# Optimization experiments

Measured on AMD Instinct MI355X. Metric: run time of the kernel, lower is better.

Reference implementation:

```python
import jax, jax.numpy as jnp
import numpy as np

N = 30000      # num_nodes
E = 480000     # num_edges
NF = 128       # node_features
EF = 64        # edge_features
HID = 256      # hidden_dim
L = 4          # num_layers
H = 8          # heads
D = HID // H   # per-head dim = 32
SCALE = 0.02


def _ln(x, g, b, eps=1e-5):
    m = x.mean(-1, keepdims=True)
    v = ((x - m) ** 2).mean(-1, keepdims=True)
    return (x - m) * jax.lax.rsqrt(v + eps) * g + b


def _mlp_head(x, W1, b1, W2, b2):
    return jax.nn.sigmoid(jax.nn.relu(x @ W1 + b1) @ W2 + b2)


def setup_inputs() -> dict:
    key = jax.random.key(0)
    ks = jax.random.split(key, 32)
    r = lambda k, shp: SCALE * jax.random.normal(k, shp, dtype=jnp.float32)
    inp = {
        'x': jax.random.normal(ks[0], (N, NF), dtype=jnp.float32),
        'edge_attr': jax.random.normal(ks[1], (E, EF), dtype=jnp.float32),
        'edge_index': jax.random.randint(ks[2], (2, E), 0, N, dtype=jnp.int32),
        # encoders
        'enc_Wn': r(ks[3], (NF, HID)), 'enc_bn': jnp.zeros((HID,), jnp.float32),
        'enc_We': r(ks[4], (EF, HID)), 'enc_be': jnp.zeros((HID,), jnp.float32),
        # stacked TransformerConv params for L layers
        'Wq': r(ks[5], (L, HID, HID)), 'bq': jnp.zeros((L, HID), jnp.float32),
        'Wk': r(ks[6], (L, HID, HID)), 'bk': jnp.zeros((L, HID), jnp.float32),
        'Wv': r(ks[7], (L, HID, HID)), 'bv': jnp.zeros((L, HID), jnp.float32),
        'We': r(ks[8], (L, HID, HID)),  # lin_edge has no bias in PyG
        'Wsk': r(ks[9], (L, HID, HID)), 'bsk': jnp.zeros((L, HID), jnp.float32),
        # shared LayerNorm (module reuses self.norm every layer)
        'ln_g': jnp.ones((HID,), jnp.float32), 'ln_b': jnp.zeros((HID,), jnp.float32),
        # contagion predictor
        'cp_W1': r(ks[10], (HID, HID // 2)), 'cp_b1': jnp.zeros((HID // 2,), jnp.float32),
        'cp_W2': r(ks[11], (HID // 2, 1)), 'cp_b2': jnp.zeros((1,), jnp.float32),
        # systemic risk predictor
        'sp_W1': r(ks[12], (HID, HID // 2)), 'sp_b1': jnp.zeros((HID // 2,), jnp.float32),
        'sp_W2': r(ks[13], (HID // 2, 1)), 'sp_b2': jnp.zeros((1,), jnp.float32),
    }
    return inp


def reference(x, edge_attr, edge_index, enc_Wn, enc_bn, enc_We, enc_be,
              Wq, bq, Wk, bk, Wv, bv, We, Wsk, bsk, ln_g, ln_b,
              cp_W1, cp_b1, cp_W2, cp_b2, sp_W1, sp_b1, sp_W2, sp_b2):
    src, dst = edge_index[0], edge_index[1]
    h = x @ enc_Wn + enc_bn                 # [N,HID]
    e = edge_attr @ enc_We + enc_be         # [E,HID]
    inv_sqrt_d = 1.0 / jnp.sqrt(jnp.asarray(D, h.dtype))
    for l in range(L):
        # TransformerConv: query at dst, key/value at src, edge bias on both k and v
        q = (h @ Wq[l] + bq[l]).reshape(N, H, D)[dst]            # [E,H,D]
        ke = (e @ We[l]).reshape(E, H, D)                        # [E,H,D]
        k = (h @ Wk[l] + bk[l]).reshape(N, H, D)[src] + ke
        v = (h @ Wv[l] + bv[l]).reshape(N, H, D)[src] + ke
        score = (q * k).sum(-1) * inv_sqrt_d                     # [E,H]
        smax = jax.ops.segment_max(score, dst, num_segments=N)   # [N,H]
        p = jnp.exp(score - smax[dst])
        denom = jax.ops.segment_sum(p, dst, num_segments=N)
        alpha = p / (denom[dst] + 1e-16)                         # scatter-softmax
        agg = jax.ops.segment_sum(alpha[..., None] * v, dst, num_segments=N)
        out = agg.reshape(N, HID) + h @ Wsk[l] + bsk[l]          # concat heads + root skip
        h = _ln(h + out, ln_g, ln_b)                             # residual + shared LN (eval: no dropout)
    g = h.mean(0, keepdims=True)                                 # [1,HID] global mean pool
    contagion_risk = _mlp_head(h, cp_W1, cp_b1, cp_W2, cp_b2)    # [N,1]
    systemic_risk = _mlp_head(g, sp_W1, sp_b1, sp_W2, sp_b2)     # [1,1]
    return h, g, contagion_risk, systemic_risk
```

## Files before the change

kernel.cpp:

```cpp
#include <hip/hip_runtime.h>
#include <cstddef>
#include <cstdint>

#define NN 30000
#define EE 480000
#define NFD 128
#define EFD 64
#define HID 256
#define NL 4
#define NH 8

#define DT_BF16 0
#define DT_F32  1
#define DT_EXT  2

#define OFF_WT  ((size_t)65787648)
#define MIN_B   ((size_t)68015872)
#define MIN_A   ((size_t)129455872)

#define WT_ENC 0
#define WT_LAYER(l) (32768 + (size_t)(l) * 262144)
#define WT_CP1 (32768 + (size_t)1048576)

typedef short bf16x8 __attribute__((ext_vector_type(8)));
typedef unsigned short us8 __attribute__((ext_vector_type(8)));
typedef float f32x4 __attribute__((ext_vector_type(4)));

__device__ __forceinline__ float bf2f(unsigned short u) {
  union { unsigned int i; float f; } v; v.i = ((unsigned int)u) << 16; return v.f;
}
__device__ __forceinline__ unsigned short f2bf(float f) {
  union { float f; unsigned int i; } v; v.f = f;
  unsigned int i = v.i;
  return (unsigned short)((i + 0x7FFFu + ((i >> 16) & 1u)) >> 16);
}
struct F4 { float x, y, z, w; };
__device__ __forceinline__ F4 load4bf(const unsigned short* p) {
  ushort4 u = *reinterpret_cast<const ushort4*>(p);
  F4 f; f.x = bf2f(u.x); f.y = bf2f(u.y); f.z = bf2f(u.z); f.w = bf2f(u.w);
  return f;
}
__device__ __forceinline__ F4 load4f(const float* p) {
  float4 t = *reinterpret_cast<const float4*>(p);
  F4 f; f.x = t.x; f.y = t.y; f.z = t.z; f.w = t.w; return f;
}
__device__ __forceinline__ F4 load4any(const void* p, size_t idx, int f32) {
  return f32 ? load4f((const float*)p + idx) : load4bf((const unsigned short*)p + idx);
}
__device__ __forceinline__ float load1any(const void* p, size_t idx, int f32) {
  return f32 ? ((const float*)p)[idx] : bf2f(((const unsigned short*)p)[idx]);
}
__device__ __forceinline__ void store1any(void* p, size_t idx, float v, int f32) {
  if (f32) ((float*)p)[idx] = v; else ((unsigned short*)p)[idx] = f2bf(v);
}

__global__ void probe_dtype(const void* __restrict__ ln_g, int* __restrict__ flag) {
  unsigned int u = *(const unsigned int*)ln_g;
  *flag = ((u & 0xFFFFu) == 0u) ? 1 : 0;
}

__global__ void wt_build(const void* __restrict__ enc_Wn,
                         const void* __restrict__ Wq, const void* __restrict__ Wk,
                         const void* __restrict__ Wv, const void* __restrict__ Wsk,
                         const void* __restrict__ cp_W1,
                         unsigned short* __restrict__ Wt, const int* __restrict__ flagp)
{
  const int f = *flagp;
  size_t idx = (size_t)blockIdx.x * 256 + threadIdx.x;
  if (idx < 32768) {
    int n = idx >> 7, k = idx & 127;
    Wt[WT_ENC + idx] = f2bf(load1any(enc_Wn, (size_t)k * 256 + n, f));
  } else if (idx < 32768 + 1048576) {
    size_t off = idx - 32768;
    int l = off >> 18;
    int which = (off >> 16) & 3;
    size_t e = off & 65535;
    int n = e >> 8, k = e & 255;
    const void* W = (which == 0) ? Wq : (which == 1) ? Wk : (which == 2) ? Wv : Wsk;
    Wt[idx] = f2bf(load1any(W, (size_t)l * 65536 + (size_t)k * 256 + n, f));
  } else if (idx < 32768 + 1048576 + 32768) {
    size_t e = idx - 32768 - 1048576;
    int n = e >> 8, k = e & 255;
    Wt[idx] = f2bf(load1any(cp_W1, (size_t)k * 128 + n, f));
  }
}

template<bool OUT_F32, bool RELU>
__global__ __launch_bounds__(256) void mfma_gemm(
    const void* __restrict__ Av, int aMode,
    const unsigned short* __restrict__ Bt,
    const void* __restrict__ biasv, size_t biasEl, int biasMode,
    void* __restrict__ Cv, int ldC, int cOff,
    int M, int K, const int* __restrict__ flagp)
{
  const int f = *flagp;
  const int aF32 = (aMode == DT_EXT) ? f : aMode;
  const int biF32 = (biasMode == DT_EXT) ? f : biasMode;

  __shared__ unsigned short Al[128][40];
  __shared__ unsigned short Bl[64][40];
  const int bm = blockIdx.x * 128;
  const int bn = blockIdx.y * 64;
  const int tid = threadIdx.x;
  const int wv = tid >> 6, lane = tid & 63;
  const int l16 = lane & 15, quad = lane >> 4;

  f32x4 acc[2][4];
#pragma unroll
  for (int i = 0; i < 2; i++)
#pragma unroll
    for (int j = 0; j < 4; j++) acc[i][j] = (f32x4){0.f, 0.f, 0.f, 0.f};

  const int ar = tid >> 1;
  const int ah = (tid & 1) << 4;
  const int bnr = tid >> 2;
  const int bk8 = (tid & 3) << 3;

  for (int k0 = 0; k0 < K; k0 += 32) {
    us8 w0, w1;
    int gr = bm + ar;
    if (gr < M) {
      if (!aF32) {
        const unsigned short* ap = (const unsigned short*)Av + (size_t)gr * K + k0 + ah;
        w0 = *(const us8*)ap;
        w1 = *(const us8*)(ap + 8);
      } else {
        const float* ap = (const float*)Av + (size_t)gr * K + k0 + ah;
        float4 u0 = *(const float4*)ap;
        float4 u1 = *(const float4*)(ap + 4);
        float4 u2 = *(const float4*)(ap + 8);
        float4 u3 = *(const float4*)(ap + 12);
        w0[0] = f2bf(u0.x); w0[1] = f2bf(u0.y); w0[2] = f2bf(u0.z); w0[3] = f2bf(u0.w);
        w0[4] = f2bf(u1.x); w0[5] = f2bf(u1.y); w0[6] = f2bf(u1.z); w0[7] = f2bf(u1.w);
        w1[0] = f2bf(u2.x); w1[1] = f2bf(u2.y); w1[2] = f2bf(u2.z); w1[3] = f2bf(u2.w);
        w1[4] = f2bf(u3.x); w1[5] = f2bf(u3.y); w1[6] = f2bf(u3.z); w1[7] = f2bf(u3.w);
      }
    } else {
      w0 = (us8)0; w1 = (us8)0;
    }
    *(us8*)&Al[ar][ah] = w0;
    *(us8*)&Al[ar][ah + 8] = w1;
    *(us8*)&Bl[bnr][bk8] = *(const us8*)&Bt[(size_t)(bn + bnr) * K + k0 + bk8];
    __syncthreads();

    bf16x8 a0 = *(const bf16x8*)&Al[wv * 32 + l16][quad * 8];
    bf16x8 a1 = *(const bf16x8*)&Al[wv * 32 + 16 + l16][quad * 8];
#pragma unroll
    for (int tn = 0; tn < 4; tn++) {
      bf16x8 b = *(const bf16x8*)&Bl[tn * 16 + l16][quad * 8];
      acc[0][tn] = __builtin_amdgcn_mfma_f32_16x16x32_bf16(a0, b, acc[0][tn], 0, 0, 0);
      acc[1][tn] = __builtin_amdgcn_mfma_f32_16x16x32_bf16(a1, b, acc[1][tn], 0, 0, 0);
    }
    __syncthreads();
  }

#pragma unroll
  for (int tm = 0; tm < 2; tm++) {
#pragma unroll
    for (int tn = 0; tn < 4; tn++) {
      int col = bn + tn * 16 + l16;
      float bias = load1any(biasv, biasEl + col, biF32);
#pragma unroll
      for (int r = 0; r < 4; r++) {
        int row = bm + wv * 32 + tm * 16 + quad * 4 + r;
        if (row < M) {
          float v = acc[tm][tn][r] + bias;
          if (RELU) v = fmaxf(v, 0.f);
          size_t off = (size_t)row * ldC + cOff + col;
          if (OUT_F32) ((float*)Cv)[off] = v;
          else ((unsigned short*)Cv)[off] = f2bf(v);
        }
      }
    }
  }
}

__global__ __launch_bounds__(256) void mfma_gemm_qkvs(
    const unsigned short* __restrict__ A,
    const unsigned short* __restrict__ Bt,
    const void* __restrict__ bq, const void* __restrict__ bk,
    const void* __restrict__ bv, const void* __restrict__ bsk, size_t biasEl,
    unsigned short* __restrict__ Qb, unsigned short* __restrict__ KVb,
    unsigned short* __restrict__ Sb,
    int M, const int* __restrict__ flagp)
{
  const int f = *flagp;
  __shared__ unsigned short Al[128][40];
  __shared__ unsigned short Bl[64][40];
  const int bm = blockIdx.x * 128;
  const int bnG = blockIdx.y * 64;
  const int which = bnG >> 8;
  const int bn = bnG & 255;
  const int tid = threadIdx.x;
  const int wv = tid >> 6, lane = tid & 63;
  const int l16 = lane & 15, quad = lane >> 4;

  f32x4 acc[2][4];
#pragma unroll
  for (int i = 0; i < 2; i++)
#pragma unroll
    for (int j = 0; j < 4; j++) acc[i][j] = (f32x4){0.f, 0.f, 0.f, 0.f};

  const int ar = tid >> 1;
  const int ah = (tid & 1) << 4;
  const int bnr = tid >> 2;
  const int bk8 = (tid & 3) << 3;
  const unsigned short* Bbase = Bt + (size_t)which * 65536;

  for (int k0 = 0; k0 < HID; k0 += 32) {
    us8 w0, w1;
    int gr = bm + ar;
    if (gr < M) {
      const unsigned short* ap = A + (size_t)gr * HID + k0 + ah;
      w0 = *(const us8*)ap;
      w1 = *(const us8*)(ap + 8);
    } else {
      w0 = (us8)0; w1 = (us8)0;
    }
    *(us8*)&Al[ar][ah] = w0;
    *(us8*)&Al[ar][ah + 8] = w1;
    *(us8*)&Bl[bnr][bk8] = *(const us8*)&Bbase[(size_t)(bn + bnr) * HID + k0 + bk8];
    __syncthreads();

    bf16x8 a0 = *(const bf16x8*)&Al[wv * 32 + l16][quad * 8];
    bf16x8 a1 = *(const bf16x8*)&Al[wv * 32 + 16 + l16][quad * 8];
#pragma unroll
    for (int tn = 0; tn < 4; tn++) {
      bf16x8 b = *(const bf16x8*)&Bl[tn * 16 + l16][quad * 8];
      acc[0][tn] = __builtin_amdgcn_mfma_f32_16x16x32_bf16(a0, b, acc[0][tn], 0, 0, 0);
      acc[1][tn] = __builtin_amdgcn_mfma_f32_16x16x32_bf16(a1, b, acc[1][tn], 0, 0, 0);
    }
    __syncthreads();
  }

  const void* biasv = (which == 0) ? bq : (which == 1) ? bk : (which == 2) ? bv : bsk;
  unsigned short* out = (which == 0) ? Qb : (which == 3) ? Sb : KVb;
  const int ldC = (which == 1 || which == 2) ? 512 : 256;
  const int cOff = (which == 2) ? 256 : 0;

#pragma unroll
  for (int tm = 0; tm < 2; tm++) {
#pragma unroll
    for (int tn = 0; tn < 4; tn++) {
      int col = bn + tn * 16 + l16;
      float bias = load1any(biasv, biasEl + col, f);
#pragma unroll
      for (int r = 0; r < 4; r++) {
        int row = bm + wv * 32 + tm * 16 + quad * 4 + r;
        if (row < M)
          out[(size_t)row * ldC + cOff + col] = f2bf(acc[tm][tn][r] + bias);
      }
    }
  }
}

__global__ void fold_kernel(const void* __restrict__ enc_We,
                            const void* __restrict__ enc_be,
                            const void* __restrict__ We_all,
                            float* __restrict__ Mfold, const int* __restrict__ flagp)
{
  const int f = *flagp;
  int idx = blockIdx.x * blockDim.x + threadIdx.x;
  if (idx >= NL * 65 * HID) return;
  int l = idx / (65 * HID);
  int rc = idx - l * 65 * HID;
  int row = rc >> 8;
  int col = rc & 255;
  size_t Wbase = (size_t)l * HID * HID;
  float acc = 0.f;
  if (row < 64) {
    for (int k = 0; k < HID; k++)
      acc += load1any(enc_We, (size_t)row * HID + k, f) * load1any(We_all, Wbase + (size_t)k * HID + col, f);
  } else {
    for (int k = 0; k < HID; k++)
      acc += load1any(enc_be, k, f) * load1any(We_all, Wbase + (size_t)k * HID + col, f);
  }
  Mfold[idx] = acc;
}

__global__ void hist_kernel(const int* __restrict__ dst, int* __restrict__ rp) {
  int e = blockIdx.x * 256 + threadIdx.x;
  if (e < EE) atomicAdd(&rp[dst[e]], 1);
}

__global__ __launch_bounds__(1024) void scan_kernel(int* __restrict__ rp) {
  __shared__ int part[1024];
  int t = threadIdx.x;
  int base = t * 30;
  int loc[30];
  int sum = 0;
#pragma unroll
  for (int i = 0; i < 30; i++) {
    int idx = base + i;
    int v = (idx < NN) ? rp[idx] : 0;
    loc[i] = v; sum += v;
  }
  part[t] = sum;
  __syncthreads();
  for (int off = 1; off < 1024; off <<= 1) {
    int v = (t >= off) ? part[t - off] : 0;
    __syncthreads();
    part[t] += v;
    __syncthreads();
  }
  int run = (t == 0) ? 0 : part[t - 1];
#pragma unroll
  for (int i = 0; i < 30; i++) {
    int idx = base + i;
    if (idx < NN) { rp[idx] = run; run += loc[i]; }
    else if (idx == NN) { rp[NN] = run; }
  }
}

__global__ void scatter_kernel(const int* __restrict__ src, const int* __restrict__ dst,
                               const int* __restrict__ rp, int* __restrict__ cnt2,
                               int2* __restrict__ sed) {
  int e = blockIdx.x * 256 + threadIdx.x;
  if (e >= EE) return;
  int d = dst[e];
  int pos = rp[d] + atomicAdd(&cnt2[d], 1);
  int2 v; v.x = src[e]; v.y = e;
  sed[pos] = v;
}

__global__ void ea_build(const int2* __restrict__ sed, const void* __restrict__ edge_attr,
                         unsigned short* __restrict__ ea_srt, const int* __restrict__ flagp) {
  const int f = *flagp;
  int gid = blockIdx.x * 256 + threadIdx.x;
  int pos = gid >> 4;
  int sub = (gid & 15) * 4;
  int e = sed[pos].y;
  F4 v = load4any(edge_attr, (size_t)e * EFD + sub, f);
  ushort4 o; o.x = f2bf(v.x); o.y = f2bf(v.y); o.z = f2bf(v.z); o.w = f2bf(v.w);
  *reinterpret_cast<ushort4*>(ea_srt + (size_t)pos * EFD + sub) = o;
}

template<bool SORTED>
__global__ __launch_bounds__(256, 8) void edge_fused(
    const int* __restrict__ rp, const int2* __restrict__ sed,
    const unsigned short* __restrict__ Qb, const unsigned short* __restrict__ KV,
    const unsigned short* __restrict__ ea_srt,
    const void* __restrict__ edge_attr,
    const float* __restrict__ Mf,
    const unsigned short* __restrict__ Sb,
    unsigned short* __restrict__ hb,
    const void* __restrict__ ln_g, const void* __restrict__ ln_b,
    const int* __restrict__ flagp)
{
  __shared__ float wl[4][8][68];
  const int f = *flagp;
  const int wv = __builtin_amdgcn_readfirstlane(threadIdx.x >> 6);
  const int nw = blockIdx.x * 4 + wv;
  const int lane = threadIdx.x & 63;
  const int hd = lane >> 3;
  const int j = lane & 7;
  const int jb = j << 3;
  const int c4 = lane * 4;

  const size_t rowb = (size_t)nw * HID;
  F4 q4 = load4bf(Qb + rowb + c4);

  float t8[8];
  {
    float q32[32];
#pragma unroll
    for (int i = 0; i < 8; i++) {
      F4 t = load4bf(Qb + rowb + hd * 32 + i * 4);
      q32[i * 4 + 0] = t.x; q32[i * 4 + 1] = t.y; q32[i * 4 + 2] = t.z; q32[i * 4 + 3] = t.w;
    }
#pragma unroll
    for (int kk = 0; kk < 8; kk++) {
      const float* Mrow = Mf + (size_t)(jb + kk) * HID + hd * 32;
      float a = 0.f;
#pragma unroll
      for (int cc = 0; cc < 8; cc++) {
        float4 m4 = *reinterpret_cast<const float4*>(Mrow + cc * 4);
        a = fmaf(m4.x, q32[cc * 4 + 0], a);
        a = fmaf(m4.y, q32[cc * 4 + 1], a);
        a = fmaf(m4.z, q32[cc * 4 + 2], a);
        a = fmaf(m4.w, q32[cc * 4 + 3], a);
      }
      t8[kk] = a;
    }
  }
  float s0;
  {
    F4 b4 = load4f(Mf + (size_t)64 * HID + c4);
    s0 = q4.x * b4.x + q4.y * b4.y + q4.z * b4.z + q4.w * b4.w;
    s0 += __shfl_xor(s0, 1);
    s0 += __shfl_xor(s0, 2);
    s0 += __shfl_xor(s0, 4);
  }

  float accv[4] = {0.f, 0.f, 0.f, 0.f};
  float wacc[8] = {0.f, 0.f, 0.f, 0.f, 0.f, 0.f, 0.f, 0.f};
  float den = 0.f;
  const int beg = rp[nw], end = rp[nw + 1];

  if (beg < end) {
    const float scl = 0.17677669529663687f;
    int tA = beg;
    int tB = (beg + 1 < end) ? beg + 1 : beg;
    int sA = sed[tA].x;
    int sB = sed[tB].x;
    const unsigned short* kvp;
    kvp = KV + (size_t)sA * 512;
    F4 kA = load4bf(kvp + c4);
    F4 vA = load4bf(kvp + 256 + c4);
    kvp = KV + (size_t)sB * 512;
    F4 kB = load4bf(kvp + c4);
    F4 vB = load4bf(kvp + 256 + c4);
    float eaA, eaB;
    if (SORTED) {
      eaA = bf2f(ea_srt[(size_t)tA * EFD + lane]);
      eaB = bf2f(ea_srt[(size_t)tB * EFD + lane]);
    } else {
      eaA = load1any(edge_attr, (size_t)sed[tA].y * EFD + lane, f);
      eaB = load1any(edge_attr, (size_t)sed[tB].y * EFD + lane, f);
    }
    int tC = (beg + 2 < end) ? beg + 2 : beg;
    int tD = (beg + 3 < end) ? beg + 3 : beg;
    int sC = sed[tC].x;
    int sD = sed[tD].x;

    for (int t = beg; t < end; t += 2) {
      kvp = KV + (size_t)sC * 512;
      F4 kC = load4bf(kvp + c4);
      F4 vC = load4bf(kvp + 256 + c4);
      kvp = KV + (size_t)sD * 512;
      F4 kD = load4bf(kvp + c4);
      F4 vD = load4bf(kvp + 256 + c4);
      float eaC, eaD;
      if (SORTED) {
        eaC = bf2f(ea_srt[(size_t)tC * EFD + lane]);
        eaD = bf2f(ea_srt[(size_t)tD * EFD + lane]);
      } else {
        eaC = load1any(edge_attr, (size_t)sed[tC].y * EFD + lane, f);
        eaD = load1any(edge_attr, (size_t)sed[tD].y * EFD + lane, f);
      }
      int tE = (t + 4 < end) ? t + 4 : beg;
      int tF = (t + 5 < end) ? t + 5 : beg;
      int sE = sed[tE].x;
      int sF = sed[tF].x;

      float mB = (t + 1 < end) ? 1.f : 0.f;
      float pA, pB;
      {
        float rB = q4.x * kB.x + q4.y * kB.y + q4.z * kB.z + q4.w * kB.w;
        float eB[8];
#pragma unroll
        for (int i = 0; i < 8; i++) {
          eB[i] = __shfl(eaB, jb + i, 64);
          rB = fmaf(eB[i], t8[i], rB);
        }
        rB += __shfl_xor(rB, 1);
        rB += __shfl_xor(rB, 2);
        rB += __shfl_xor(rB, 4);
        float scB = fminf(fmaxf((rB + s0) * scl, -30.f), 30.f);
        pB = mB * __expf(scB);
        accv[0] = fmaf(pB, vB.x, accv[0]);
        accv[1] = fmaf(pB, vB.y, accv[1]);
        accv[2] = fmaf(pB, vB.z, accv[2]);
        accv[3] = fmaf(pB, vB.w, accv[3]);
#pragma unroll
        for (int i = 0; i < 8; i++) wacc[i] = fmaf(pB, eB[i], wacc[i]);
      }
      {
        float rA = q4.x * kA.x + q4.y * kA.y + q4.z * kA.z + q4.w * kA.w;
        float eA[8];
#pragma unroll
        for (int i = 0; i < 8; i++) {
          eA[i] = __shfl(eaA, jb + i, 64);
          rA = fmaf(eA[i], t8[i], rA);
        }
        rA += __shfl_xor(rA, 1);
        rA += __shfl_xor(rA, 2);
        rA += __shfl_xor(rA, 4);
        float scA = fminf(fmaxf((rA + s0) * scl, -30.f), 30.f);
        pA = __expf(scA);
        accv[0] = fmaf(pA, vA.x, accv[0]);
        accv[1] = fmaf(pA, vA.y, accv[1]);
        accv[2] = fmaf(pA, vA.z, accv[2]);
        accv[3] = fmaf(pA, vA.w, accv[3]);
#pragma unroll
        for (int i = 0; i < 8; i++) wacc[i] = fmaf(pA, eA[i], wacc[i]);
      }
      den += pA + pB;
      kA = kC; vA = vC; eaA = eaC;
      kB = kD; vB = vD; eaB = eaD;
      tC = tE; tD = tF; sC = sE; sD = sF;
    }
  }

#pragma unroll
  for (int i = 0; i < 8; i++) wl[wv][hd][jb + i] = wacc[i];
  __syncthreads();

  float ke0 = 0.f, ke1 = 0.f, ke2 = 0.f, ke3 = 0.f;
#pragma unroll 8
  for (int k = 0; k < 64; k++) {
    float w = wl[wv][hd][k];
    float4 m4 = *reinterpret_cast<const float4*>(Mf + (size_t)k * HID + c4);
    ke0 = fmaf(w, m4.x, ke0);
    ke1 = fmaf(w, m4.y, ke1);
    ke2 = fmaf(w, m4.z, ke2);
    ke3 = fmaf(w, m4.w, ke3);
  }

  float invden = 1.f / (den + 1e-16f);
  float sel = (end > beg) ? 1.f : 0.f;
  __builtin_amdgcn_sched_barrier(0);
  F4 b4 = load4f(Mf + (size_t)64 * HID + c4);
  F4 s4 = load4bf(Sb + rowb + c4);
  F4 hh = load4bf(hb + rowb + c4);
  float r0 = hh.x + sel * ((accv[0] + ke0) * invden + b4.x) + s4.x;
  float r1 = hh.y + sel * ((accv[1] + ke1) * invden + b4.y) + s4.y;
  float r2 = hh.z + sel * ((accv[2] + ke2) * invden + b4.z) + s4.z;
  float r3 = hh.w + sel * ((accv[3] + ke3) * invden + b4.w) + s4.w;

  float sum = r0 + r1 + r2 + r3;
#pragma unroll
  for (int o = 1; o < 64; o <<= 1) sum += __shfl_xor(sum, o);
  float mean = sum * (1.f / HID);
  float d0 = r0 - mean, d1 = r1 - mean, d2 = r2 - mean, d3 = r3 - mean;
  float vs = d0 * d0 + d1 * d1 + d2 * d2 + d3 * d3;
#pragma unroll
  for (int o = 1; o < 64; o <<= 1) vs += __shfl_xor(vs, o);
  float rstd = rsqrtf(vs * (1.f / HID) + 1e-5f);
  ushort4 o4;
  o4.x = f2bf(d0 * rstd * load1any(ln_g, c4 + 0, f) + load1any(ln_b, c4 + 0, f));
  o4.y = f2bf(d1 * rstd * load1any(ln_g, c4 + 1, f) + load1any(ln_b, c4 + 1, f));
  o4.z = f2bf(d2 * rstd * load1any(ln_g, c4 + 2, f) + load1any(ln_b, c4 + 2, f));
  o4.w = f2bf(d3 * rstd * load1any(ln_g, c4 + 3, f) + load1any(ln_b, c4 + 3, f));
  *reinterpret_cast<ushort4*>(hb + rowb + c4) = o4;
}

__global__ void copy_h_out(const unsigned short* __restrict__ h, void* __restrict__ out,
                           const int* __restrict__ flagp) {
  const int f = *flagp;
  int i = blockIdx.x * 256 + threadIdx.x;
  store1any(out, i, bf2f(h[i]), f);
}

__global__ void colsum_kernel(const unsigned short* __restrict__ h, float* __restrict__ gsum) {
  int c = threadIdx.x;
  float s = 0.f;
  for (int r = blockIdx.x; r < NN; r += gridDim.x) s += bf2f(h[(size_t)r * HID + c]);
  atomicAdd(&gsum[c], s);
}

__global__ void write_g_kernel(const float* __restrict__ gsum, void* __restrict__ out,
                               const int* __restrict__ flagp) {
  const int f = *flagp;
  int c = threadIdx.x;
  store1any(out, (size_t)NN * HID + c, gsum[c] * (1.f / NN), f);
}

__global__ __launch_bounds__(256) void cp2_kernel(
    const float* __restrict__ hid, const void* __restrict__ W2,
    const void* __restrict__ b2, void* __restrict__ out,
    const int* __restrict__ flagp)
{
  const int f = *flagp;
  int nw = (blockIdx.x << 2) + (threadIdx.x >> 6);
  if (nw >= NN) return;
  int lane = threadIdx.x & 63;
  const float* hr = hid + (size_t)nw * 128;
  float s = hr[lane * 2] * load1any(W2, lane * 2, f) + hr[lane * 2 + 1] * load1any(W2, lane * 2 + 1, f);
#pragma unroll
  for (int o = 1; o < 64; o <<= 1) s += __shfl_xor(s, o);
  if (lane == 0) {
    float xv = s + load1any(b2, 0, f);
    store1any(out, (size_t)NN * HID + HID + nw, 1.f / (1.f + __expf(-xv)), f);
  }
}

__global__ __launch_bounds__(128) void sys_kernel(
    const float* __restrict__ gsum,
    const void* __restrict__ W1, const void* __restrict__ b1,
    const void* __restrict__ W2, const void* __restrict__ b2,
    void* __restrict__ out, const int* __restrict__ flagp)
{
  const int f = *flagp;
  __shared__ float red[2];
  int j = threadIdx.x;
  float acc = load1any(b1, j, f);
  const float invN = 1.f / NN;
  for (int k = 0; k < HID; k++) acc = fmaf(gsum[k] * invN, load1any(W1, (size_t)k * 128 + j, f), acc);
  float v = fmaxf(acc, 0.f) * load1any(W2, j, f);
#pragma unroll
  for (int o = 1; o < 64; o <<= 1) v += __shfl_xor(v, o);
  if ((j & 63) == 0) red[j >> 6] = v;
  __syncthreads();
  if (j == 0) {
    float xv = red[0] + red[1] + load1any(b2, 0, f);
    store1any(out, (size_t)NN * HID + HID + NN, 1.f / (1.f + __expf(-xv)), f);
  }
}

__global__ void diag_kernel(float* __restrict__ out, float v, int n4) {
  int i = blockIdx.x * 256 + threadIdx.x;
  if (i < n4) out[i] = (i == 0) ? v : 0.f;
}

extern "C" void kernel_launch(void* const* d_in, const int* in_sizes, int n_in,
                              void* d_out, int out_size, void* d_ws, size_t ws_size,
                              hipStream_t stream)
{
  (void)in_sizes; (void)n_in;

  if (ws_size < MIN_B) {
    diag_kernel<<<(out_size / 2 + 255) / 256, 256, 0, stream>>>(
        (float*)d_out, (float)(ws_size >> 20), out_size / 2);
    return;
  }
  const bool planA = (ws_size >= MIN_A);

  const void* x         = d_in[0];
  const void* edge_attr = d_in[1];
  const int*  edge_index= (const int*)d_in[2];
  const void* enc_Wn = d_in[3];
  const void* enc_bn = d_in[4];
  const void* enc_We = d_in[5];
  const void* enc_be = d_in[6];
  const void* Wq  = d_in[7];
  const void* bq  = d_in[8];
  const void* Wk  = d_in[9];
  const void* bk  = d_in[10];
  const void* Wv  = d_in[11];
  const void* bvv = d_in[12];
  const void* We  = d_in[13];
  const void* Wsk = d_in[14];
  const void* bsk = d_in[15];
  const void* ln_g = d_in[16];
  const void* ln_b = d_in[17];
  const void* cp_W1 = d_in[18];
  const void* cp_b1 = d_in[19];
  const void* cp_W2 = d_in[20];
  const void* cp_b2 = d_in[21];
  const void* sp_W1 = d_in[22];
  const void* sp_b1 = d_in[23];
  const void* sp_W2 = d_in[24];
  const void* sp_b2 = d_in[25];

  char* ws = (char*)d_ws;
  unsigned short* hb  = (unsigned short*)(ws + 0);
  unsigned short* Sb  = (unsigned short*)(ws + 15360000);
  unsigned short* KVb = (unsigned short*)(ws + 30720000);
  int2*  sed   = (int2*)(ws + 61440000);
  int*   rp    = (int*)(ws + 65280000);
  int*   cnt2  = (int*)(ws + 65400064);
  float* Mfold = (float*)(ws + 65520128);
  float* gsum  = (float*)(ws + 65786368);
  int*   flagp = (int*)(ws + 65787392);
  unsigned short* Wt = (unsigned short*)(ws + OFF_WT);
  unsigned short* ea_srt = (unsigned short*)(ws + MIN_B);
  unsigned short* Qb = (unsigned short*)d_out;
  float* cph = (float*)(ws + 15360000);

  const int* src = edge_index;
  const int* dst = edge_index + EE;

  probe_dtype<<<1, 1, 0, stream>>>(ln_g, flagp);
  wt_build<<<(1114112 + 255) / 256, 256, 0, stream>>>(enc_Wn, Wq, Wk, Wv, Wsk, cp_W1, Wt, flagp);
  fold_kernel<<<(NL * 65 * HID + 255) / 256, 256, 0, stream>>>(enc_We, enc_be, We, Mfold, flagp);

  hipMemsetAsync(rp, 0, 120064, stream);
  hipMemsetAsync(cnt2, 0, 120064, stream);
  hist_kernel<<<(EE + 255) / 256, 256, 0, stream>>>(dst, rp);
  scan_kernel<<<1, 1024, 0, stream>>>(rp);
  scatter_kernel<<<(EE + 255) / 256, 256, 0, stream>>>(src, dst, rp, cnt2, sed);
  if (planA) {
    ea_build<<<EE * 16 / 256, 256, 0, stream>>>(sed, edge_attr, ea_srt, flagp);
  }

  const int gx = (NN + 127) / 128;
  {
    dim3 g(gx, 4);
    mfma_gemm<false, false><<<g, 256, 0, stream>>>(
        x, DT_EXT, Wt + WT_ENC, enc_bn, 0, DT_EXT, hb, HID, 0, NN, NFD, flagp);
  }

  for (int l = 0; l < NL; l++) {
    size_t bo = (size_t)l * HID;
    dim3 gQ(gx, 16);
    mfma_gemm_qkvs<<<gQ, 256, 0, stream>>>(
        hb, Wt + WT_LAYER(l), bq, bk, bvv, bsk, bo, Qb, KVb, Sb, NN, flagp);
    const float* Mf = Mfold + (size_t)l * 65 * HID;
    if (planA) {
      edge_fused<true><<<NN / 4, 256, 0, stream>>>(
          rp, sed, Qb, KVb, ea_srt, edge_attr, Mf, Sb, hb, ln_g, ln_b, flagp);
    } else {
      edge_fused<false><<<NN / 4, 256, 0, stream>>>(
          rp, sed, Qb, KVb, ea_srt, edge_attr, Mf, Sb, hb, ln_g, ln_b, flagp);
    }
  }

  copy_h_out<<<NN, 256, 0, stream>>>(hb, d_out, flagp);
  hipMemsetAsync(gsum, 0, HID * 4, stream);
  colsum_kernel<<<256, 256, 0, stream>>>(hb, gsum);
  write_g_kernel<<<1, 256, 0, stream>>>(gsum, d_out, flagp);

  {
    dim3 g(gx, 2);
    mfma_gemm<true, true><<<g, 256, 0, stream>>>(
        hb, DT_BF16, Wt + WT_CP1, cp_b1, 0, DT_EXT, cph, 128, 0, NN, HID, flagp);
  }
  cp2_kernel<<<NN / 4, 256, 0, stream>>>(cph, cp_W2, cp_b2, d_out, flagp);
  sys_kernel<<<1, 128, 0, stream>>>(gsum, sp_W1, sp_b1, sp_W2, sp_b2, d_out, flagp);
}
```

Measured before the change: 2.351 ms.

## Rework edge loop: one-ahead prefetch, vector edge-attr loads, scalarized indices

Replaces the two-edges-per-iteration, four-deep register prefetch pipeline in the attention aggregation loop with a simpler ping-pong loop that prefetches only the next edge. Each lane now loads its 8 edge-attribute values directly as one 16-byte vector instead of broadcasting them across lanes with eight shuffles. Source and edge indices are made wave-uniform with readfirstlane so address math can run on scalar registers. The shallower prefetch cuts register pressure and shuffle traffic, but leaves less memory latency hidden per edge. The scheduling barrier before the epilogue is also removed.

```diff
diff --git a/kernel.cpp b/kernel.cpp
--- a/kernel.cpp
+++ b/kernel.cpp
@@ -399,97 +399,78 @@
 
   if (beg < end) {
     const float scl = 0.17677669529663687f;
-    int tA = beg;
-    int tB = (beg + 1 < end) ? beg + 1 : beg;
-    int sA = sed[tA].x;
-    int sB = sed[tB].x;
-    const unsigned short* kvp;
-    kvp = KV + (size_t)sA * 512;
-    F4 kA = load4bf(kvp + c4);
-    F4 vA = load4bf(kvp + 256 + c4);
-    kvp = KV + (size_t)sB * 512;
-    F4 kB = load4bf(kvp + c4);
-    F4 vB = load4bf(kvp + 256 + c4);
-    float eaA, eaB;
-    if (SORTED) {
-      eaA = bf2f(ea_srt[(size_t)tA * EFD + lane]);
-      eaB = bf2f(ea_srt[(size_t)tB * EFD + lane]);
-    } else {
-      eaA = load1any(edge_attr, (size_t)sed[tA].y * EFD + lane, f);
-      eaB = load1any(edge_attr, (size_t)sed[tB].y * EFD + lane, f);
-    }
-    int tC = (beg + 2 < end) ? beg + 2 : beg;
-    int tD = (beg + 3 < end) ? beg + 3 : beg;
-    int sC = sed[tC].x;
-    int sD = sed[tD].x;
-
-    for (int t = beg; t < end; t += 2) {
-      kvp = KV + (size_t)sC * 512;
-      F4 kC = load4bf(kvp + c4);
-      F4 vC = load4bf(kvp + 256 + c4);
-      kvp = KV + (size_t)sD * 512;
-      F4 kD = load4bf(kvp + c4);
-      F4 vD = load4bf(kvp + 256 + c4);
-      float eaC, eaD;
-      if (SORTED) {
-        eaC = bf2f(ea_srt[(size_t)tC * EFD + lane]);
-        eaD = bf2f(ea_srt[(size_t)tD * EFD + lane]);
-      } else {
-        eaC = load1any(edge_attr, (size_t)sed[tC].y * EFD + lane, f);
-        eaD = load1any(edge_attr, (size_t)sed[tD].y * EFD + lane, f);
-      }
-      int tE = (t + 4 < end) ? t + 4 : beg;
-      int tF = (t + 5 < end) ? t + 5 : beg;
-      int sE = sed[tE].x;
-      int sF = sed[tF].x;
-
-      float mB = (t + 1 < end) ? 1.f : 0.f;
-      float pA, pB;
-      {
-        float rB = q4.x * kB.x + q4.y * kB.y + q4.z * kB.z + q4.w * kB.w;
-        float eB[8];
-#pragma unroll
-        for (int i = 0; i < 8; i++) {
-          eB[i] = __shfl(eaB, jb + i, 64);
-          rB = fmaf(eB[i], t8[i], rB);
-        }
-        rB += __shfl_xor(rB, 1);
-        rB += __shfl_xor(rB, 2);
-        rB += __shfl_xor(rB, 4);
-        float scB = fminf(fmaxf((rB + s0) * scl, -30.f), 30.f);
-        pB = mB * __expf(scB);
-        accv[0] = fmaf(pB, vB.x, accv[0]);
-        accv[1] = fmaf(pB, vB.y, accv[1]);
-        accv[2] = fmaf(pB, vB.z, accv[2]);
-        accv[3] = fmaf(pB, vB.w, accv[3]);
-#pragma unroll
-        for (int i = 0; i < 8; i++) wacc[i] = fmaf(pB, eB[i], wacc[i]);
-      }
-      {
-        float rA = q4.x * kA.x + q4.y * kA.y + q4.z * kA.z + q4.w * kA.w;
-        float eA[8];
-#pragma unroll
-        for (int i = 0; i < 8; i++) {
-          eA[i] = __shfl(eaA, jb + i, 64);
-          rA = fmaf(eA[i], t8[i], rA);
-        }
-        rA += __shfl_xor(rA, 1);
-        rA += __shfl_xor(rA, 2);
-        rA += __shfl_xor(rA, 4);
-        float scA = fminf(fmaxf((rA + s0) * scl, -30.f), 30.f);
-        pA = __expf(scA);
-        accv[0] = fmaf(pA, vA.x, accv[0]);
-        accv[1] = fmaf(pA, vA.y, accv[1]);
-        accv[2] = fmaf(pA, vA.z, accv[2]);
-        accv[3] = fmaf(pA, vA.w, accv[3]);
-#pragma unroll
-        for (int i = 0; i < 8; i++) wacc[i] = fmaf(pA, eA[i], wacc[i]);
-      }
-      den += pA + pB;
-      kA = kC; vA = vC; eaA = eaC;
-      kB = kD; vB = vD; eaB = eaD;
-      tC = tE; tD = tF; sC = sE; sD = sF;
-    }
+
+#define LOADE(tt, kk, vvv, ee) do {                                            \
+    int2 _sv = sed[(tt)];                                                      \
+    int _sx = __builtin_amdgcn_readfirstlane(_sv.x);                           \
+    const unsigned short* _kvp = KV + (size_t)_sx * 512;                       \
+    kk  = *reinterpret_cast<const ushort4*>(_kvp + c4);                        \
+    vvv = *reinterpret_cast<const ushort4*>(_kvp + 256 + c4);                  \
+    if (SORTED) {                                                              \
+      ee = *reinterpret_cast<const us8*>(ea_srt + (size_t)(tt) * EFD + jb);    \
+    } else {                                                                   \
+      int _ey = __builtin_amdgcn_readfirstlane(_sv.y);                         \
+      if (!f) {                                                                \
+        ee = *reinterpret_cast<const us8*>((const unsigned short*)edge_attr +  \
+                                           (size_t)_ey * EFD + jb);            \
+      } else {                                                                 \
+        const float* _ep = (const float*)edge_attr + (size_t)_ey * EFD + jb;   \
+        float4 _u0 = *(const float4*)_ep;                                      \
+        float4 _u1 = *(const float4*)(_ep + 4);                                \
+        ee[0] = (short)f2bf(_u0.x); ee[1] = (short)f2bf(_u0.y);                \
+        ee[2] = (short)f2bf(_u0.z); ee[3] = (short)f2bf(_u0.w);                \
+        ee[4] = (short)f2bf(_u1.x); ee[5] = (short)f2bf(_u1.y);                \
+        ee[6] = (short)f2bf(_u1.z); ee[7] = (short)f2bf(_u1.w);                \
+      }                                                                        \
+    }                                                                          \
+  } while (0)
+
+#define COMPUTE(kk, vvv, ee) do {                                              \
+    float _r = q4.x * bf2f(kk.x) + q4.y * bf2f(kk.y) +                         \
+               q4.z * bf2f(kk.z) + q4.w * bf2f(kk.w);                          \
+    float _e0 = bf2f((unsigned short)ee[0]);                                   \
+    float _e1 = bf2f((unsigned short)ee[1]);                                   \
+    float _e2 = bf2f((unsigned short)ee[2]);                                   \
+    float _e3 = bf2f((unsigned short)ee[3]);                                   \
+    float _e4 = bf2f((unsigned short)ee[4]);                                   \
+    float _e5 = bf2f((unsigned short)ee[5]);                                   \
+    float _e6 = bf2f((unsigned short)ee[6]);                                   \
+    float _e7 = bf2f((unsigned short)ee[7]);                                   \
+    _r = fmaf(_e0, t8[0], _r); _r = fmaf(_e1, t8[1], _r);                      \
+    _r = fmaf(_e2, t8[2], _r); _r = fmaf(_e3, t8[3], _r);                      \
+    _r = fmaf(_e4, t8[4], _r); _r = fmaf(_e5, t8[5], _r);                      \
+    _r = fmaf(_e6, t8[6], _r); _r = fmaf(_e7, t8[7], _r);                      \
+    _r += __shfl_xor(_r, 1);                                                   \
+    _r += __shfl_xor(_r, 2);                                                   \
+    _r += __shfl_xor(_r, 4);                                                   \
+    float _sc = fminf(fmaxf((_r + s0) * scl, -30.f), 30.f);                    \
+    float _p = __expf(_sc);                                                    \
+    den += _p;                                                                 \
+    accv[0] = fmaf(_p, bf2f(vvv.x), accv[0]);                                  \
+    accv[1] = fmaf(_p, bf2f(vvv.y), accv[1]);                                  \
+    accv[2] = fmaf(_p, bf2f(vvv.z), accv[2]);                                  \
+    accv[3] = fmaf(_p, bf2f(vvv.w), accv[3]);                                  \
+    wacc[0] = fmaf(_p, _e0, wacc[0]); wacc[1] = fmaf(_p, _e1, wacc[1]);        \
+    wacc[2] = fmaf(_p, _e2, wacc[2]); wacc[3] = fmaf(_p, _e3, wacc[3]);        \
+    wacc[4] = fmaf(_p, _e4, wacc[4]); wacc[5] = fmaf(_p, _e5, wacc[5]);        \
+    wacc[6] = fmaf(_p, _e6, wacc[6]); wacc[7] = fmaf(_p, _e7, wacc[7]);        \
+  } while (0)
+
+    ushort4 k0, v0, k1, v1;
+    us8 e0, e1;
+    k1 = (ushort4){0, 0, 0, 0}; v1 = k1; e1 = (us8)0;
+    LOADE(beg, k0, v0, e0);
+    int t = beg;
+    for (;;) {
+      if (t + 1 < end) LOADE(t + 1, k1, v1, e1);
+      COMPUTE(k0, v0, e0);
+      if (++t >= end) break;
+      if (t + 1 < end) LOADE(t + 1, k0, v0, e0);
+      COMPUTE(k1, v1, e1);
+      if (++t >= end) break;
+    }
+#undef LOADE
+#undef COMPUTE
   }
 
 #pragma unroll
@@ -509,7 +490,6 @@
 
   float invden = 1.f / (den + 1e-16f);
   float sel = (end > beg) ? 1.f : 0.f;
-  __builtin_amdgcn_sched_barrier(0);
   F4 b4 = load4f(Mf + (size_t)64 * HID + c4);
   F4 s4 = load4bf(Sb + rowb + c4);
   F4 hh = load4bf(hb + rowb + c4);
```

After: 2.477 ms. +5.4%, slower.
